# Optimization experiments

Measured on AMD Instinct MI355X. Metric: run time of the kernel, lower is better.

The kernel has to match this reference:

```python
import jax, jax.numpy as jnp
import numpy as np

B, H = 65536, 19


def _nbr(x):
    # 4-neighbor sum, equivalent to conv2d with cross kernel [[0,1,0],[1,0,1],[0,1,0]], padding=1
    p = jnp.pad(x, ((0, 0), (1, 1), (1, 1)))
    return p[:, :-2, 1:-1] + p[:, 2:, 1:-1] + p[:, 1:-1, :-2] + p[:, 1:-1, 2:]


def setup_inputs() -> dict:
    key = jax.random.key(0)
    k1, k2, k3 = jax.random.split(key, 3)
    # ternary board: 0 empty, 1 black, 2 white -> disjoint stone planes
    board = jax.random.randint(k1, (B, H, H), 0, 3)
    stones = jnp.stack([(board == 1), (board == 2)], axis=1).astype(jnp.float32)  # [B,2,H,H]
    current_player = jax.random.randint(k2, (B,), 0, 2, dtype=jnp.int32)
    ko_points = jax.random.randint(k3, (B, 2), 0, H, dtype=jnp.int32)  # all kos active (>=0)
    return {"stones": stones, "current_player": current_player, "ko_points": ko_points}


def reference(stones, current_player, ko_points):
    f32 = jnp.float32
    cp = current_player[:, None, None]  # [B,1,1]
    cur = jnp.where(cp == 0, stones[:, 0], stones[:, 1])  # [B,H,H] float 0/1
    opp = jnp.where(cp == 0, stones[:, 1], stones[:, 0])
    empty = 1.0 - stones[:, 0] - stones[:, 1]             # float 0/1 (planes disjoint)
    empty_b = empty > 0.5

    # legal_moves()
    legal = empty_b & (_nbr(empty) > 0)
    opp_lib = _nbr(opp)
    weak = (opp > 0.5) & (opp_lib == 1)
    adj_weak = _nbr(weak.astype(f32)) > 0
    legal = legal | (empty_b & adj_weak)
    ids = jnp.arange(stones.shape[0])
    has_ko = ko_points[:, 0] >= 0
    rr = jnp.clip(ko_points[:, 0], 0, H - 1)
    cc = jnp.clip(ko_points[:, 1], 0, H - 1)
    legal = legal.at[ids, rr, cc].set(jnp.where(has_ko, False, legal[ids, rr, cc]))

    cur_lib = _nbr(cur) * empty
    turn = jnp.broadcast_to(current_player.astype(f32)[:, None, None], (stones.shape[0], H, H))
    return jnp.stack([cur, opp, legal.astype(f32), cur_lib, turn], axis=1)  # [B,5,H,H]
```

## Files before the change

kernel.cpp:

```cpp
#include <hip/hip_runtime.h>

#define GO_H 19
#define NCELL 361
#define G 4
#define NIN (G * 2 * NCELL)
#define NC_G (G * NCELL)

__global__ __launch_bounds__(256) void go_features_kernel(
    const float* __restrict__ stones,
    const int*   __restrict__ cur_player,
    const int*   __restrict__ ko,
    float*       __restrict__ out,
    int B)
{
    __shared__ float sarr[NIN];
    __shared__ float weak_s[NC_G];
    __shared__ int   cp_s[G];
    __shared__ int   koc_s[G];
    __shared__ int   opp_off_s[G];

    const int tid = threadIdx.x;
    const int gb  = blockIdx.x * G;

    {
        const float4* in4 = (const float4*)(stones + (size_t)gb * (2 * NCELL));
        float4* s4 = (float4*)sarr;
        #pragma unroll
        for (int i = tid; i < NIN / 4; i += 256) s4[i] = in4[i];
    }

    if (tid < G) {
        int b  = gb + tid;
        int cp = cur_player[b];
        cp_s[tid] = cp;
        opp_off_s[tid] = tid * (2 * NCELL) + (cp == 0 ? NCELL : 0);
        int kr = ko[2 * b], kc = ko[2 * b + 1];
        int rr = min(max(kr, 0), GO_H - 1);
        int cc = min(max(kc, 0), GO_H - 1);
        koc_s[tid] = (kr >= 0) ? (rr * GO_H + cc) : -1;
    }
    __syncthreads();

    for (int i = tid; i < NC_G; i += 256) {
        int g   = i / NCELL;
        int c   = i - g * NCELL;
        int r   = c / GO_H;
        int col = c - r * GO_H;
        int ob  = opp_off_s[g];

        float mu = (r > 0)          ? 1.f : 0.f;
        float md = (r < GO_H - 1)   ? 1.f : 0.f;
        float ml = (col > 0)        ? 1.f : 0.f;
        float mr = (col < GO_H - 1) ? 1.f : 0.f;
        int iu = (r > 0)          ? c - GO_H : c;
        int id = (r < GO_H - 1)   ? c + GO_H : c;
        int il = (col > 0)        ? c - 1    : c;
        int ir = (col < GO_H - 1) ? c + 1    : c;

        float opl = sarr[ob + iu] * mu + sarr[ob + id] * md
                  + sarr[ob + il] * ml + sarr[ob + ir] * mr;
        float osf = sarr[ob + c];
        weak_s[i] = (osf > 0.5f && opl == 1.0f) ? 1.f : 0.f;
    }
    __syncthreads();

    for (int i = tid; i < NC_G; i += 256) {
        int g   = i / NCELL;
        int c   = i - g * NCELL;
        int r   = c / GO_H;
        int col = c - r * GO_H;
        int base = g * (2 * NCELL);
        int cp   = cp_s[g];
        int wb   = g * NCELL;

        float mu = (r > 0)          ? 1.f : 0.f;
        float md = (r < GO_H - 1)   ? 1.f : 0.f;
        float ml = (col > 0)        ? 1.f : 0.f;
        float mr = (col < GO_H - 1) ? 1.f : 0.f;
        int iu = (r > 0)          ? c - GO_H : c;
        int id = (r < GO_H - 1)   ? c + GO_H : c;
        int il = (col > 0)        ? c - 1    : c;
        int ir = (col < GO_H - 1) ? c + 1    : c;

        float s0 = sarr[base + c];
        float s1 = sarr[base + NCELL + c];
        float cu = cp ? s1 : s0;
        float op = cp ? s0 : s1;
        float em = 1.f - s0 - s1;

        float ne = 0.f, ncur = 0.f;
        {
            float n0, n1;
            n0 = sarr[base + iu]; n1 = sarr[base + NCELL + iu];
            ne += (1.f - n0 - n1) * mu;  ncur += (cp ? n1 : n0) * mu;
            n0 = sarr[base + id]; n1 = sarr[base + NCELL + id];
            ne += (1.f - n0 - n1) * md;  ncur += (cp ? n1 : n0) * md;
            n0 = sarr[base + il]; n1 = sarr[base + NCELL + il];
            ne += (1.f - n0 - n1) * ml;  ncur += (cp ? n1 : n0) * ml;
            n0 = sarr[base + ir]; n1 = sarr[base + NCELL + ir];
            ne += (1.f - n0 - n1) * mr;  ncur += (cp ? n1 : n0) * mr;
        }
        float nw = weak_s[wb + iu] * mu + weak_s[wb + id] * md
                 + weak_s[wb + il] * ml + weak_s[wb + ir] * mr;

        bool emb   = em > 0.5f;
        bool legal = emb && (ne > 0.f || nw > 0.f);
        if (c == koc_s[g]) legal = false;

        size_t obase = (size_t)(gb + g) * (5 * NCELL);
        out[obase + c]             = cu;
        out[obase + NCELL + c]     = op;
        out[obase + 2 * NCELL + c] = legal ? 1.f : 0.f;
        out[obase + 3 * NCELL + c] = ncur * em;
        out[obase + 4 * NCELL + c] = (float)cp;
    }
}

extern "C" void kernel_launch(void* const* d_in, const int* in_sizes, int n_in,
                              void* d_out, int out_size, void* d_ws, size_t ws_size,
                              hipStream_t stream) {
    const float* stones     = (const float*)d_in[0];
    const int*   cur_player = (const int*)d_in[1];
    const int*   ko         = (const int*)d_in[2];
    float*       out        = (float*)d_out;

    const int B = in_sizes[1];
    const int nblocks = B / G;
    go_features_kernel<<<nblocks, 256, 0, stream>>>(stones, cur_player, ko, out, B);
}
```

Before: 586.1 us.

## Bit-pack board rows and compute neighbor counts with bitwise adders, stage output in LDS

Each board row is packed into 19-bit masks per thread (76 threads per block of 4 boards). The neighbor sums, weak-group detection and liberty counts are then computed with shift/xor/and bit-adder logic instead of per-cell float stencils. Outputs are staged in shared memory and written back with coalesced float4 stores instead of scattered scalar stores. This cuts ALU and LDS work and improves store coalescing, but only 76 of 256 threads do the compute phases and the per-row unpack loops are serial.

```diff
diff --git a/kernel.cpp b/kernel.cpp
--- a/kernel.cpp
+++ b/kernel.cpp
@@ -1,10 +1,12 @@
 #include <hip/hip_runtime.h>
 
-#define GO_H 19
-#define NCELL 361
-#define G 4
-#define NIN (G * 2 * NCELL)
-#define NC_G (G * NCELL)
+#define GO_H   19
+#define NCELL  361
+#define G      4
+#define NROWS  (G * GO_H)
+#define MASK19 0x7FFFFu
+#define OUTF   (G * 5 * NCELL)
+#define INF4   ((G * 2 * NCELL) / 4)
 
 __global__ __launch_bounds__(256) void go_features_kernel(
     const float* __restrict__ stones,
@@ -13,106 +15,104 @@
     float*       __restrict__ out,
     int B)
 {
-    __shared__ float sarr[NIN];
-    __shared__ float weak_s[NC_G];
-    __shared__ int   cp_s[G];
-    __shared__ int   koc_s[G];
-    __shared__ int   opp_off_s[G];
+    __shared__ __align__(16) float out_s[OUTF];
+    __shared__ unsigned c_m[G][GO_H];
+    __shared__ unsigned o_m[G][GO_H];
+    __shared__ unsigned e_m[G][GO_H];
+    __shared__ unsigned w_m[G][GO_H];
+    __shared__ float    cpf_s[G];
+    __shared__ int      kor_s[G];
+    __shared__ unsigned kcm_s[G];
 
     const int tid = threadIdx.x;
     const int gb  = blockIdx.x * G;
 
     {
         const float4* in4 = (const float4*)(stones + (size_t)gb * (2 * NCELL));
-        float4* s4 = (float4*)sarr;
-        #pragma unroll
-        for (int i = tid; i < NIN / 4; i += 256) s4[i] = in4[i];
-    }
-
-    if (tid < G) {
-        int b  = gb + tid;
-        int cp = cur_player[b];
-        cp_s[tid] = cp;
-        opp_off_s[tid] = tid * (2 * NCELL) + (cp == 0 ? NCELL : 0);
-        int kr = ko[2 * b], kc = ko[2 * b + 1];
-        int rr = min(max(kr, 0), GO_H - 1);
-        int cc = min(max(kc, 0), GO_H - 1);
-        koc_s[tid] = (kr >= 0) ? (rr * GO_H + cc) : -1;
+        float4* s4 = (float4*)out_s;
+        for (int i = tid; i < INF4; i += 256) s4[i] = in4[i];
     }
     __syncthreads();
 
-    for (int i = tid; i < NC_G; i += 256) {
-        int g   = i / NCELL;
-        int c   = i - g * NCELL;
-        int r   = c / GO_H;
-        int col = c - r * GO_H;
-        int ob  = opp_off_s[g];
-
-        float mu = (r > 0)          ? 1.f : 0.f;
-        float md = (r < GO_H - 1)   ? 1.f : 0.f;
-        float ml = (col > 0)        ? 1.f : 0.f;
-        float mr = (col < GO_H - 1) ? 1.f : 0.f;
-        int iu = (r > 0)          ? c - GO_H : c;
-        int id = (r < GO_H - 1)   ? c + GO_H : c;
-        int il = (col > 0)        ? c - 1    : c;
-        int ir = (col < GO_H - 1) ? c + 1    : c;
-
-        float opl = sarr[ob + iu] * mu + sarr[ob + id] * md
-                  + sarr[ob + il] * ml + sarr[ob + ir] * mr;
-        float osf = sarr[ob + c];
-        weak_s[i] = (osf > 0.5f && opl == 1.0f) ? 1.f : 0.f;
+    unsigned c = 0, o = 0, e = 0;
+    int g = 0, r = 0;
+    if (tid < NROWS) {
+        g = tid / GO_H;
+        r = tid - g * GO_H;
+        const int b  = gb + g;
+        const int cp = cur_player[b];
+        const float* bp = out_s + g * (2 * NCELL) + r * GO_H;
+        unsigned p0 = 0, p1 = 0;
+        #pragma unroll
+        for (int j = 0; j < GO_H; ++j) {
+            if (bp[j] > 0.5f)         p0 |= 1u << j;
+            if (bp[NCELL + j] > 0.5f) p1 |= 1u << j;
+        }
+        c = cp ? p1 : p0;
+        o = cp ? p0 : p1;
+        e = ~(p0 | p1) & MASK19;
+        c_m[g][r] = c;  o_m[g][r] = o;  e_m[g][r] = e;
+        if (r == 0) {
+            cpf_s[g] = (float)cp;
+            int kr = ko[2 * b], kc = ko[2 * b + 1];
+            int rr = min(max(kr, 0), GO_H - 1);
+            int cc = min(max(kc, 0), GO_H - 1);
+            kor_s[g] = (kr >= 0) ? rr : -1;
+            kcm_s[g] = 1u << cc;
+        }
     }
     __syncthreads();
 
-    for (int i = tid; i < NC_G; i += 256) {
-        int g   = i / NCELL;
-        int c   = i - g * NCELL;
-        int r   = c / GO_H;
-        int col = c - r * GO_H;
-        int base = g * (2 * NCELL);
-        int cp   = cp_s[g];
-        int wb   = g * NCELL;
+    unsigned w = 0, legal_nw = 0, l0 = 0, l1 = 0, l2 = 0;
+    if (tid < NROWS) {
+        unsigned oU = r ? o_m[g][r-1] : 0u;
+        unsigned oD = (r < GO_H-1) ? o_m[g][r+1] : 0u;
+        unsigned a  = (o << 1) & MASK19, bq = o >> 1;
+        unsigned x1  = a ^ bq ^ oU ^ oD;
+        unsigned at2 = (a & bq) | (oU & oD) | ((a | bq) & (oU | oD));
+        w = o & x1 & ~at2;
+        w_m[g][r] = w;
 
-        float mu = (r > 0)          ? 1.f : 0.f;
-        float md = (r < GO_H - 1)   ? 1.f : 0.f;
-        float ml = (col > 0)        ? 1.f : 0.f;
-        float mr = (col < GO_H - 1) ? 1.f : 0.f;
-        int iu = (r > 0)          ? c - GO_H : c;
-        int id = (r < GO_H - 1)   ? c + GO_H : c;
-        int il = (col > 0)        ? c - 1    : c;
-        int ir = (col < GO_H - 1) ? c + 1    : c;
+        unsigned eU = r ? e_m[g][r-1] : 0u;
+        unsigned eD = (r < GO_H-1) ? e_m[g][r+1] : 0u;
+        legal_nw = e & ((e << 1) | (e >> 1) | eU | eD);
 
-        float s0 = sarr[base + c];
-        float s1 = sarr[base + NCELL + c];
-        float cu = cp ? s1 : s0;
-        float op = cp ? s0 : s1;
-        float em = 1.f - s0 - s1;
+        unsigned cU = r ? c_m[g][r-1] : 0u;
+        unsigned cD = (r < GO_H-1) ? c_m[g][r+1] : 0u;
+        unsigned ca = (c << 1) & MASK19, cb = c >> 1;
+        unsigned s1 = ca ^ cb, k1 = ca & cb;
+        unsigned s2 = s1 ^ cU, k2 = s1 & cU;
+        unsigned s3 = s2 ^ cD, k3 = s2 & cD;
+        l0 = s3 & e;
+        l1 = (k1 ^ k2 ^ k3) & e;
+        l2 = ((k1 & k2) | (k1 & k3) | (k2 & k3)) & e;
+    }
+    __syncthreads();
 
-        float ne = 0.f, ncur = 0.f;
-        {
-            float n0, n1;
-            n0 = sarr[base + iu]; n1 = sarr[base + NCELL + iu];
-            ne += (1.f - n0 - n1) * mu;  ncur += (cp ? n1 : n0) * mu;
-            n0 = sarr[base + id]; n1 = sarr[base + NCELL + id];
-            ne += (1.f - n0 - n1) * md;  ncur += (cp ? n1 : n0) * md;
-            n0 = sarr[base + il]; n1 = sarr[base + NCELL + il];
-            ne += (1.f - n0 - n1) * ml;  ncur += (cp ? n1 : n0) * ml;
-            n0 = sarr[base + ir]; n1 = sarr[base + NCELL + ir];
-            ne += (1.f - n0 - n1) * mr;  ncur += (cp ? n1 : n0) * mr;
+    if (tid < NROWS) {
+        unsigned wU = r ? w_m[g][r-1] : 0u;
+        unsigned wD = (r < GO_H-1) ? w_m[g][r+1] : 0u;
+        unsigned legal = legal_nw | (e & (((w << 1) & MASK19) | (w >> 1) | wU | wD));
+        if (r == kor_s[g]) legal &= ~kcm_s[g];
+        const float cpf = cpf_s[g];
+        float* ob = out_s + g * (5 * NCELL) + r * GO_H;
+        #pragma unroll
+        for (int j = 0; j < GO_H; ++j) {
+            ob[j]             = (float)((c >> j) & 1u);
+            ob[NCELL + j]     = (float)((o >> j) & 1u);
+            ob[2 * NCELL + j] = (float)((legal >> j) & 1u);
+            ob[3 * NCELL + j] = (float)(((l0 >> j) & 1u) |
+                                        (((l1 >> j) & 1u) << 1) |
+                                        (((l2 >> j) & 1u) << 2));
+            ob[4 * NCELL + j] = cpf;
         }
-        float nw = weak_s[wb + iu] * mu + weak_s[wb + id] * md
-                 + weak_s[wb + il] * ml + weak_s[wb + ir] * mr;
+    }
+    __syncthreads();
 
-        bool emb   = em > 0.5f;
-        bool legal = emb && (ne > 0.f || nw > 0.f);
-        if (c == koc_s[g]) legal = false;
-
-        size_t obase = (size_t)(gb + g) * (5 * NCELL);
-        out[obase + c]             = cu;
-        out[obase + NCELL + c]     = op;
-        out[obase + 2 * NCELL + c] = legal ? 1.f : 0.f;
-        out[obase + 3 * NCELL + c] = ncur * em;
-        out[obase + 4 * NCELL + c] = (float)cp;
+    {
+        const float4* s4 = (const float4*)out_s;
+        float4* o4 = (float4*)(out + (size_t)gb * (5 * NCELL));
+        for (int i = tid; i < OUTF / 4; i += 256) o4[i] = s4[i];
     }
 }
 
```

New measurement: 586.9 us. No clear change (+0.1%).
